# Kernel optimization log

Hardware: AMD Instinct MI355X
Metric: run time of the kernel (lower is better)

The kernel has to match this reference:

```python
import jax, jax.numpy as jnp
import numpy as np

NUM_HEADS = 16
DIM = 1024
HARMONICS = 32
B, L = 2, 2048


def holo_linear(x, basis, phase, amp):
    # x: [B,L,in]; basis: [H,in] (L2-normalized rows); phase/amp: [out,H]
    # Original builds complex(res,0) * amp*exp(i*phase) and takes real of sum
    # over harmonics -> sum_h res_h * amp[o,h]*cos(phase[o,h]).
    resonance = jnp.einsum('bli,hi->blh', x, basis)        # [B,L,H]
    w = amp * jnp.cos(phase)                               # [out,H]
    return jnp.einsum('blh,oh->blo', resonance, w)         # [B,L,out]


def setup_inputs() -> dict:
    key = jax.random.key(0)
    ks = jax.random.split(key, 13)
    two_pi = 2.0 * np.pi

    def make_proj(k0, k1):
        basis = jax.random.normal(k0, (HARMONICS, DIM), dtype=jnp.float32)
        basis = basis / jnp.linalg.norm(basis, axis=1, keepdims=True)
        phase = jax.random.normal(k1, (DIM, HARMONICS), dtype=jnp.float32) * two_pi
        amp = jnp.ones((DIM, HARMONICS), dtype=jnp.float32) / HARMONICS
        return basis, phase, amp

    x = jax.random.normal(ks[0], (B, L, DIM), dtype=jnp.float32)
    bq, pq, aq = make_proj(ks[1], ks[2])
    bk, pk, ak = make_proj(ks[3], ks[4])
    bv, pv, av = make_proj(ks[5], ks[6])
    bo, po, ao = make_proj(ks[7], ks[8])
    return {
        'x': x,
        'basis_q': bq, 'phase_q': pq, 'amp_q': aq,
        'basis_k': bk, 'phase_k': pk, 'amp_k': ak,
        'basis_v': bv, 'phase_v': pv, 'amp_v': av,
        'basis_o': bo, 'phase_o': po, 'amp_o': ao,
    }


def reference(x, basis_q, phase_q, amp_q, basis_k, phase_k, amp_k,
              basis_v, phase_v, amp_v, basis_o, phase_o, amp_o):
    Bsz, Ls, C = x.shape
    head_dim = C // NUM_HEADS
    scale = head_dim ** (-0.5)

    def split_heads(t):  # [B,L,C] -> [B,H,L,hd]
        return t.reshape(Bsz, Ls, NUM_HEADS, head_dim).transpose(0, 2, 1, 3)

    q = split_heads(holo_linear(x, basis_q, phase_q, amp_q))
    k = split_heads(holo_linear(x, basis_k, phase_k, amp_k))
    v = split_heads(holo_linear(x, basis_v, phase_v, amp_v))

    attn = jnp.einsum('bhqd,bhkd->bhqk', q, k) * scale      # [B,H,L,L]
    attn = jax.nn.softmax(attn, axis=-1)
    out = jnp.einsum('bhqk,bhkd->bhqd', attn, v)            # [B,H,L,hd]
    out = out.transpose(0, 2, 1, 3).reshape(Bsz, Ls, C)
    return holo_linear(out, basis_o, phase_o, amp_o)
```

## Files before the change

kernel.cpp:

```cpp
#include <hip/hip_runtime.h>
#include <hip/hip_bf16.h>
#include <cstdint>
#include <cstddef>

#define NH   16
#define HD   64
#define CD   1024
#define HARM 32
#define BSZ  2
#define LSEQ 2048
#define NROW (BSZ*LSEQ)

typedef __attribute__((ext_vector_type(8))) short short8;
typedef __attribute__((ext_vector_type(16))) float float16v;

__device__ inline ushort bf16u(float f) {
    __hip_bfloat16 h = __float2bfloat16(f);
    return *(ushort*)&h;
}
__device__ inline float ubf(ushort u) {
    return __uint_as_float((unsigned)u << 16);
}
__device__ inline unsigned pk2(float a, float b) {
    return (unsigned)bf16u(a) | ((unsigned)bf16u(b) << 16);
}
__device__ inline int crow(int r, int half) { return (r & 3) + 8 * (r >> 2) + 4 * half; }

union S8U { short8 v; uint2 u[2]; };

__device__ inline short8 pk_frag(const unsigned* pk, int cc) {
    S8U o;
    o.u[0] = make_uint2(pk[4 * cc + 0], pk[4 * cc + 1]);
    o.u[1] = make_uint2(pk[4 * cc + 2], pk[4 * cc + 3]);
    return o.v;
}

__global__ void prep_kern(const float* __restrict__ bq, const float* __restrict__ bk,
                          const float* __restrict__ bv, const float* __restrict__ bo,
                          const float* __restrict__ pq, const float* __restrict__ aq,
                          const float* __restrict__ pk, const float* __restrict__ ak,
                          const float* __restrict__ pv, const float* __restrict__ av,
                          const float* __restrict__ po, const float* __restrict__ ao,
                          ushort* __restrict__ bF, ushort* __restrict__ wqkvF,
                          ushort* __restrict__ wobF) {
    const float QSCALE = 0.125f * 1.44269504088896340736f;
    unsigned tid = blockIdx.x * 256 + threadIdx.x;
    if (tid < 16384) {
        unsigned l31 = tid & 31, h = (tid >> 5) & 1, kc = (tid >> 6) & 63, proj = tid >> 12;
        const float* bp = (proj == 0) ? bq : (proj == 1) ? bk : (proj == 2) ? bv : bo;
        const float* s = bp + (size_t)l31 * CD + kc * 16;
        unsigned o0 = (proj == 3) ? h * 4 : h * 8;
        unsigned o1 = o0 + ((proj == 3) ? 8 : 4);
        float4 f0 = *(const float4*)(s + o0), f1 = *(const float4*)(s + o1);
        S8U o;
        o.u[0] = make_uint2(pk2(f0.x, f0.y), pk2(f0.z, f0.w));
        o.u[1] = make_uint2(pk2(f1.x, f1.y), pk2(f1.z, f1.w));
        *(short8*)(bF + (size_t)tid * 8) = o.v;
        return;
    }
    if (tid < 28672) {
        unsigned i = tid - 16384;
        unsigned l31 = i & 31, h = (i >> 5) & 1, kc2 = (i >> 6) & 1;
        unsigned ntp = (i >> 7) & 31, proj = i >> 12;
        const float* ph = (proj == 0) ? pq : (proj == 1) ? pk : pv;
        const float* am = (proj == 0) ? aq : (proj == 1) ? ak : av;
        float sc = (proj == 0) ? QSCALE : 1.0f;
        size_t s = (size_t)(ntp * 32 + l31) * HARM + kc2 * 16 + h * 4;
        float4 p0 = *(const float4*)(ph + s), p1 = *(const float4*)(ph + s + 8);
        float4 a0 = *(const float4*)(am + s), a1 = *(const float4*)(am + s + 8);
        S8U o;
        o.u[0] = make_uint2(pk2(a0.x * cosf(p0.x) * sc, a0.y * cosf(p0.y) * sc),
                            pk2(a0.z * cosf(p0.z) * sc, a0.w * cosf(p0.w) * sc));
        o.u[1] = make_uint2(pk2(a1.x * cosf(p1.x) * sc, a1.y * cosf(p1.y) * sc),
                            pk2(a1.z * cosf(p1.z) * sc, a1.w * cosf(p1.w) * sc));
        *(short8*)(wqkvF + (size_t)i * 8) = o.v;
        return;
    }
    {
        unsigned i = tid - 28672;
        unsigned l31 = i & 31, h = (i >> 5) & 1, kc2 = (i >> 6) & 1, nt = i >> 7;
        size_t s = (size_t)(nt * 32 + l31) * HARM + kc2 * 16 + h * 4;
        float4 p0 = *(const float4*)(po + s), p1 = *(const float4*)(po + s + 8);
        float4 a0 = *(const float4*)(ao + s), a1 = *(const float4*)(ao + s + 8);
        S8U o;
        o.u[0] = make_uint2(pk2(a0.x * cosf(p0.x), a0.y * cosf(p0.y)),
                            pk2(a0.z * cosf(p0.z), a0.w * cosf(p0.w)));
        o.u[1] = make_uint2(pk2(a1.x * cosf(p1.x), a1.y * cosf(p1.y)),
                            pk2(a1.z * cosf(p1.z), a1.w * cosf(p1.w)));
        *(short8*)(wobF + (size_t)i * 8) = o.v;
    }
}

__global__ __launch_bounds__(512) void resrp_kern(const float* __restrict__ x,
                                                  const ushort* __restrict__ bF,
                                                  unsigned* __restrict__ rfbuf) {
    __shared__ ushort xs[4][8192];
    float* red = (float*)xs;
    const int t = threadIdx.x, wave = t >> 6, lane = t & 63;
    const int l31 = lane & 31, h = lane >> 5;
    const int rest = blockIdx.x;
    const int n0 = rest * 32;

#pragma unroll
    for (int i = 0; i < 16; i++) {
        int idx = i * 512 + t;
        int row = idx >> 8, c4g = idx & 255;
        int kseg = c4g >> 6, c4 = c4g & 63;
        float4 v = *(const float4*)(x + (size_t)(n0 + row) * CD + kseg * 256 + c4 * 4);
        int chunk = (c4 >> 1) ^ (row & 15), sub = c4 & 1;
        *(ushort4*)(&xs[kseg][row * 256 + chunk * 8 + sub * 4]) =
            make_ushort4(bf16u(v.x), bf16u(v.y), bf16u(v.z), bf16u(v.w));
    }
    __syncthreads();

    float16v resC[3] = {};
#pragma unroll
    for (int i = 0; i < 8; i++) {
        int kcg = wave * 8 + i;
        int kseg = kcg >> 4, m = kcg & 15;
        int c = m * 2 + h;
        short8 bx = *(const short8*)(&xs[kseg][l31 * 256 + ((c ^ (l31 & 15)) * 8)]);
#pragma unroll
        for (int p = 0; p < 3; p++) {
            short8 a = *(const short8*)(bF + ((size_t)((p * 64 + kcg) * 2 + h) * 32 + l31) * 8);
            resC[p] = __builtin_amdgcn_mfma_f32_32x32x16_bf16(a, bx, resC[p], 0, 0, 0);
        }
    }

    unsigned* ob = rfbuf + (size_t)rest * 1536;
    for (int p = 0; p < 3; p++) {
        __syncthreads();
#pragma unroll
        for (int r = 0; r < 16; r++) red[wave * 1024 + r * 64 + lane] = resC[p][r];
        __syncthreads();
        if (t < 128) {
            int cc = t >> 6, ln = t & 63;
            unsigned w[4];
#pragma unroll
            for (int q = 0; q < 4; q++) {
                int j = cc * 4 + q;
                float va = 0.0f, vb2 = 0.0f;
#pragma unroll
                for (int wv = 0; wv < 8; wv++) {
                    va  += red[wv * 1024 + (2 * j) * 64 + ln];
                    vb2 += red[wv * 1024 + (2 * j + 1) * 64 + ln];
                }
                w[q] = pk2(va, vb2);
            }
            *(uint4*)(ob + ((p * 2 + cc) * 64 + ln) * 4) =
                make_uint4(w[0], w[1], w[2], w[3]);
        }
    }
}

__global__ __launch_bounds__(256) void qkv_kern(const unsigned* __restrict__ rfbuf,
                                                const ushort* __restrict__ wqkvF,
                                                ushort* __restrict__ qtile,
                                                ushort* __restrict__ ktile,
                                                ushort* __restrict__ vtile) {
    const int t = threadIdx.x, wave = t >> 6, lane = t & 63;
    const int l31 = lane & 31, h = lane >> 5;
    const int ntg = blockIdx.x % 24, rest = blockIdx.x / 24;
    const int b = rest >> 6, l0q = rest & 63;
    const int nt = ntg * 4 + wave;
    const int proj = nt >> 5, ntp = nt & 31;
    const int head = ntp >> 1, sub = ntp & 1;
    const int kblk = l0q >> 1, mtk = l0q & 1;

    const unsigned* rb = rfbuf + (size_t)rest * 1536 + ((proj * 2) * 64 + lane) * 4;
    uint4 q0 = *(const uint4*)(rb);
    uint4 q1 = *(const uint4*)(rb + 256);
    S8U r0, r1;
    r0.u[0] = make_uint2(q0.x, q0.y); r0.u[1] = make_uint2(q0.z, q0.w);
    r1.u[0] = make_uint2(q1.x, q1.y); r1.u[1] = make_uint2(q1.z, q1.w);

    const ushort* wp = wqkvF + ((size_t)(proj * 32 + ntp) * 4) * 256;
    short8 wf0 = *(const short8*)(wp + (size_t)h * 256 + l31 * 8);
    short8 wf1 = *(const short8*)(wp + (size_t)(2 + h) * 256 + l31 * 8);
    float16v c = {};
    if (proj < 2) {
        c = __builtin_amdgcn_mfma_f32_32x32x16_bf16(wf0, r0.v, c, 0, 0, 0);
        c = __builtin_amdgcn_mfma_f32_32x32x16_bf16(wf1, r1.v, c, 0, 0, 0);
    } else {
        c = __builtin_amdgcn_mfma_f32_32x32x16_bf16(r0.v, wf0, c, 0, 0, 0);
        c = __builtin_amdgcn_mfma_f32_32x32x16_bf16(r1.v, wf1, c, 0, 0, 0);
    }
    unsigned pkc[8];
#pragma unroll
    for (int j = 0; j < 8; j++) pkc[j] = pk2(c[2 * j], c[2 * j + 1]);

    if (proj == 0) {
        ushort* base = qtile + (((size_t)(b * NH + head) * 64 + l0q)) * 2048;
#pragma unroll
        for (int cc = 0; cc < 2; cc++)
            *(short8*)(base + (sub * 2 + cc) * 512 + h * 256 + l31 * 8) =
                pk_frag(pkc, cc);
    } else if (proj == 1) {
        ushort* base = ktile + ((size_t)(b * NH + head) * 32 + kblk) * 4096 + mtk * 2048;
#pragma unroll
        for (int cc = 0; cc < 2; cc++)
            *(short8*)(base + (sub * 2 + cc) * 512 + h * 256 + l31 * 8) =
                pk_frag(pkc, cc);
    } else {
        ushort* base = vtile + ((size_t)(b * NH + head) * 32 + kblk) * 4096 + sub * 2048;
#pragma unroll
        for (int cc = 0; cc < 2; cc++)
            *(short8*)(base + (mtk * 2 + cc) * 512 + h * 256 + l31 * 8) =
                pk_frag(pkc, cc);
    }
}

__global__ __launch_bounds__(256, 2) void flash8(const ushort* __restrict__ qtile,
                                                 const ushort* __restrict__ ktile,
                                                 const ushort* __restrict__ vtile,
                                                 ushort* __restrict__ Opart,
                                                 float* __restrict__ lbuf) {
    __shared__ ushort kb[2][4096];
    __shared__ ushort vb[2][4096];
    const int t = threadIdx.x;
    const int wave = t >> 6, lane = t & 63;
    const int l31 = lane & 31, h = lane >> 5;
    const int d = blockIdx.x;
    const int logical = (d & 7) * 64 + (d >> 3);
    const int bh = logical >> 4;
    const int inner = logical & 15;
    const int ksp = inner >> 3;
    const int qtg = inner & 7;
    const int qt0 = qtg * 8 + wave * 2;
    const int fo = h * 256 + l31 * 8;
    const int so = t * 8;

    const ushort* qtb = qtile + ((size_t)bh * 64 + qt0) * 2048;
    short8 qfa[4], qfb[4];
#pragma unroll
    for (int kc = 0; kc < 4; kc++) {
        qfa[kc] = *(const short8*)(qtb + kc * 512 + fo);
        qfb[kc] = *(const short8*)(qtb + 2048 + kc * 512 + fo);
    }

    const ushort* ktb = ktile + (size_t)bh * 32 * 4096;
    const ushort* vtb = vtile + (size_t)bh * 32 * 4096;
    const int k0 = ksp * 16;

    {
        const ushort* ks = ktb + (size_t)k0 * 4096;
        const ushort* vs = vtb + (size_t)k0 * 4096;
        short8 a0 = *(const short8*)(ks + so);
        short8 a1 = *(const short8*)(ks + 2048 + so);
        short8 b0 = *(const short8*)(vs + so);
        short8 b1 = *(const short8*)(vs + 2048 + so);
        *(short8*)(kb[0] + so) = a0; *(short8*)(kb[0] + 2048 + so) = a1;
        *(short8*)(vb[0] + so) = b0; *(short8*)(vb[0] + 2048 + so) = b1;
    }
    __syncthreads();

    S8U ones;
    ones.u[0] = make_uint2(0x3F803F80u, 0x3F803F80u);
    ones.u[1] = make_uint2(0x3F803F80u, 0x3F803F80u);

    float16v O0a = {}, O1a = {}, Laa = {};
    float16v O0b = {}, O1b = {}, Lab = {};

#pragma unroll
    for (int it = 0; it < 16; it++) {
        const int cur = it & 1, nxt = cur ^ 1;

        short8 a0, a1, b0, b1;
        if (it < 15) {
            const ushort* ks = ktb + (size_t)(k0 + it + 1) * 4096;
            const ushort* vs = vtb + (size_t)(k0 + it + 1) * 4096;
            a0 = *(const short8*)(ks + so);
            a1 = *(const short8*)(ks + 2048 + so);
            b0 = *(const short8*)(vs + so);
            b1 = *(const short8*)(vs + 2048 + so);
        }

        short8 kf[2][4];
#pragma unroll
        for (int mt = 0; mt < 2; mt++)
#pragma unroll
            for (int kc = 0; kc < 4; kc++)
                kf[mt][kc] = *(const short8*)(kb[cur] + mt * 2048 + kc * 512 + fo);
        float16v s0a = {}, s1a = {}, s0b = {}, s1b = {};
#pragma unroll
        for (int kc = 0; kc < 4; kc++) {
            s0a = __builtin_amdgcn_mfma_f32_32x32x16_bf16(kf[0][kc], qfa[kc], s0a, 0, 0, 0);
            s1a = __builtin_amdgcn_mfma_f32_32x32x16_bf16(kf[1][kc], qfa[kc], s1a, 0, 0, 0);
            s0b = __builtin_amdgcn_mfma_f32_32x32x16_bf16(kf[0][kc], qfb[kc], s0b, 0, 0, 0);
            s1b = __builtin_amdgcn_mfma_f32_32x32x16_bf16(kf[1][kc], qfb[kc], s1b, 0, 0, 0);
        }
        short8 vf[2][4];
#pragma unroll
        for (int mt = 0; mt < 2; mt++)
#pragma unroll
            for (int kc = 0; kc < 4; kc++)
                vf[mt][kc] = *(const short8*)(vb[cur] + mt * 2048 + kc * 512 + fo);

        unsigned pk0a[8], pk1a[8], pk0b[8], pk1b[8];
#pragma unroll
        for (int j2 = 0; j2 < 8; j2++) {
            pk0a[j2] = pk2(__builtin_amdgcn_exp2f(s0a[2 * j2]),
                           __builtin_amdgcn_exp2f(s0a[2 * j2 + 1]));
            pk1a[j2] = pk2(__builtin_amdgcn_exp2f(s1a[2 * j2]),
                           __builtin_amdgcn_exp2f(s1a[2 * j2 + 1]));
            pk0b[j2] = pk2(__builtin_amdgcn_exp2f(s0b[2 * j2]),
                           __builtin_amdgcn_exp2f(s0b[2 * j2 + 1]));
            pk1b[j2] = pk2(__builtin_amdgcn_exp2f(s1b[2 * j2]),
                           __builtin_amdgcn_exp2f(s1b[2 * j2 + 1]));
        }
#pragma unroll
        for (int kc = 0; kc < 4; kc++) {
            const unsigned* pma = (kc < 2) ? pk0a : pk1a;
            const unsigned* pmb = (kc < 2) ? pk0b : pk1b;
            short8 bfa = pk_frag(pma, kc & 1);
            short8 bfb = pk_frag(pmb, kc & 1);
            Laa = __builtin_amdgcn_mfma_f32_32x32x16_bf16(ones.v, bfa, Laa, 0, 0, 0);
            O0a = __builtin_amdgcn_mfma_f32_32x32x16_bf16(vf[0][kc], bfa, O0a, 0, 0, 0);
            O1a = __builtin_amdgcn_mfma_f32_32x32x16_bf16(vf[1][kc], bfa, O1a, 0, 0, 0);
            Lab = __builtin_amdgcn_mfma_f32_32x32x16_bf16(ones.v, bfb, Lab, 0, 0, 0);
            O0b = __builtin_amdgcn_mfma_f32_32x32x16_bf16(vf[0][kc], bfb, O0b, 0, 0, 0);
            O1b = __builtin_amdgcn_mfma_f32_32x32x16_bf16(vf[1][kc], bfb, O1b, 0, 0, 0);
        }

        if (it < 15) {
            *(short8*)(kb[nxt] + so) = a0; *(short8*)(kb[nxt] + 2048 + so) = a1;
            *(short8*)(vb[nxt] + so) = b0; *(short8*)(vb[nxt] + 2048 + so) = b1;
        }
        __syncthreads();
    }

    if (h == 0) {
        lbuf[(size_t)ksp * 65536 + bh * 2048 + qt0 * 32 + l31] = Laa[0];
        lbuf[(size_t)ksp * 65536 + bh * 2048 + (qt0 + 1) * 32 + l31] = Lab[0];
    }
#pragma unroll
    for (int j = 0; j < 2; j++) {
        ushort* ob = Opart + (size_t)ksp * 4194304 + ((size_t)bh * 64 + qt0 + j) * 2048;
#pragma unroll
        for (int mt = 0; mt < 2; mt++) {
            float16v Ov = j ? (mt ? O1b : O0b) : (mt ? O1a : O0a);
            unsigned pkO[8];
#pragma unroll
            for (int j2 = 0; j2 < 8; j2++) pkO[j2] = pk2(Ov[2 * j2], Ov[2 * j2 + 1]);
#pragma unroll
            for (int cc = 0; cc < 2; cc++)
                *(short8*)(ob + ((mt * 2 + cc) * 2 + h) * 256 + l31 * 8) =
                    pk_frag(pkO, cc);
        }
    }
}

__global__ __launch_bounds__(256) void back1_kern(const ushort* __restrict__ Opart,
                                                  const float* __restrict__ lbuf,
                                                  const ushort* __restrict__ bF,
                                                  float* __restrict__ respart2) {
    __shared__ float red[4 * 16 * 64];
    const int t = threadIdx.x, wave = t >> 6, lane = t & 63;
    const int l31 = lane & 31, h = lane >> 5;
    const int hq = blockIdx.x & 3, rg = blockIdx.x >> 2;
    const int b = rg >> 6, qt = rg & 63;
    const int hd = hq * 4 + wave, bh = b * NH + hd;

    float lb = lbuf[(size_t)bh * 2048 + qt * 32 + l31] +
               lbuf[(size_t)65536 + (size_t)bh * 2048 + qt * 32 + l31];
    float invl = 1.0f / lb;
    const ushort* ob0 = Opart + ((size_t)bh * 64 + qt) * 2048;
    const ushort* ob1 = ob0 + 4194304;

    float16v c = {};
#pragma unroll
    for (int kc = 0; kc < 4; kc++) {
        short8 o0 = *(const short8*)(ob0 + (kc * 2 + h) * 256 + l31 * 8);
        short8 o1 = *(const short8*)(ob1 + (kc * 2 + h) * 256 + l31 * 8);
        float av[8];
#pragma unroll
        for (int e = 0; e < 8; e++)
            av[e] = (ubf((ushort)o0[e]) + ubf((ushort)o1[e])) * invl;
        S8U bn;
        bn.u[0] = make_uint2(pk2(av[0], av[1]), pk2(av[2], av[3]));
        bn.u[1] = make_uint2(pk2(av[4], av[5]), pk2(av[6], av[7]));
        int kcg = hd * 4 + kc;
        short8 a = *(const short8*)(bF + ((size_t)((3 * 64 + kcg) * 2 + h) * 32 + l31) * 8);
        c = __builtin_amdgcn_mfma_f32_32x32x16_bf16(a, bn.v, c, 0, 0, 0);
    }
#pragma unroll
    for (int r = 0; r < 16; r++) red[wave * 1024 + r * 64 + lane] = c[r];
    __syncthreads();
#pragma unroll
    for (int i = 0; i < 4; i++) {
        int e = i * 256 + t;
        respart2[((size_t)hq * 128 + rg) * 1024 + e] =
            (red[e] + red[1024 + e]) + (red[2048 + e] + red[3072 + e]);
    }
}

__global__ __launch_bounds__(256) void back2_kern(const float* __restrict__ respart2,
                                                  const ushort* __restrict__ wobF,
                                                  float* __restrict__ out) {
    const int t = threadIdx.x, wave = t >> 6, lane = t & 63;
    const int l31 = lane & 31, h = lane >> 5;
    const int ng = blockIdx.x & 7, rg = blockIdx.x >> 3;

    float cf[16];
#pragma unroll
    for (int r = 0; r < 16; r++) {
        const float* pp = respart2 + r * 64 + lane;
        cf[r] = (pp[(size_t)rg * 1024] + pp[(size_t)(128 + rg) * 1024]) +
                (pp[(size_t)(256 + rg) * 1024] + pp[(size_t)(384 + rg) * 1024]);
    }
    unsigned pkr[8];
#pragma unroll
    for (int j = 0; j < 8; j++) pkr[j] = pk2(cf[2 * j], cf[2 * j + 1]);
    short8 a0 = pk_frag(pkr, 0);
    short8 a1 = pk_frag(pkr, 1);

    int nt = ng * 4 + wave;
    const ushort* wp = wobF + (size_t)nt * 1024;
    short8 wf0 = *(const short8*)(wp + (size_t)h * 256 + l31 * 8);
    short8 wf1 = *(const short8*)(wp + (size_t)(2 + h) * 256 + l31 * 8);
    float16v co = {};
    co = __builtin_amdgcn_mfma_f32_32x32x16_bf16(a0, wf0, co, 0, 0, 0);
    co = __builtin_amdgcn_mfma_f32_32x32x16_bf16(a1, wf1, co, 0, 0, 0);
#pragma unroll
    for (int r = 0; r < 16; r++) {
        int row = rg * 32 + crow(r, h);
        out[(size_t)row * CD + nt * 32 + l31] = co[r];
    }
}

extern "C" void kernel_launch(void* const* d_in, const int* in_sizes, int n_in,
                              void* d_out, int out_size, void* d_ws, size_t ws_size,
                              hipStream_t stream) {
    const float* x  = (const float*)d_in[0];
    const float* bq = (const float*)d_in[1];
    const float* pq = (const float*)d_in[2];
    const float* aq = (const float*)d_in[3];
    const float* bk = (const float*)d_in[4];
    const float* pk = (const float*)d_in[5];
    const float* ak = (const float*)d_in[6];
    const float* bv = (const float*)d_in[7];
    const float* pv = (const float*)d_in[8];
    const float* av = (const float*)d_in[9];
    const float* bo = (const float*)d_in[10];
    const float* po = (const float*)d_in[11];
    const float* ao = (const float*)d_in[12];

    char* ws = (char*)d_ws;
    ushort* bF      = (ushort*)(ws + 0);
    ushort* wqkvF   = (ushort*)(ws + 262144);
    ushort* wobF    = (ushort*)(ws + 458752);
    ushort* qtile   = (ushort*)(ws + 524288);
    ushort* ktile   = (ushort*)(ws + 8912896);
    ushort* vtile   = (ushort*)(ws + 17301504);
    ushort* Opart   = (ushort*)(ws + 25690112);
    float*  lbuf    = (float*)(ws + 42467328);
    float*  respart2= (float*)(ws + 524288);
    unsigned* rfbuf = (unsigned*)(ws + 25690112);

    prep_kern<<<128, 256, 0, stream>>>(bq, bk, bv, bo, pq, aq, pk, ak, pv, av,
                                       po, ao, bF, wqkvF, wobF);
    resrp_kern<<<128, 512, 0, stream>>>(x, bF, rfbuf);
    qkv_kern<<<3072, 256, 0, stream>>>(rfbuf, wqkvF, qtile, ktile, vtile);
    flash8<<<512, 256, 0, stream>>>(qtile, ktile, vtile, Opart, lbuf);
    back1_kern<<<512, 256, 0, stream>>>(Opart, lbuf, bF, respart2);
    back2_kern<<<1024, 256, 0, stream>>>(respart2, wobF, (float*)d_out);
}
```

Measured before the change: 151.7 us.

## Fuse back-projection kernels into one 1024-thread block per row tile

New measurement: 148.3 us. -2.2%, faster.

```diff
diff --git a/kernel.cpp b/kernel.cpp
--- a/kernel.cpp
+++ b/kernel.cpp
@@ -350,16 +350,18 @@
     }
 }
 
-__global__ __launch_bounds__(256) void back1_kern(const ushort* __restrict__ Opart,
-                                                  const float* __restrict__ lbuf,
-                                                  const ushort* __restrict__ bF,
-                                                  float* __restrict__ respart2) {
-    __shared__ float red[4 * 16 * 64];
+__global__ __launch_bounds__(1024) void backf_kern(const ushort* __restrict__ Opart,
+                                                   const float* __restrict__ lbuf,
+                                                   const ushort* __restrict__ bF,
+                                                   const ushort* __restrict__ wobF,
+                                                   float* __restrict__ out) {
+    __shared__ float red[16 * 1024];
+    __shared__ unsigned pkrL[512];
     const int t = threadIdx.x, wave = t >> 6, lane = t & 63;
     const int l31 = lane & 31, h = lane >> 5;
-    const int hq = blockIdx.x & 3, rg = blockIdx.x >> 2;
+    const int rg = blockIdx.x;
     const int b = rg >> 6, qt = rg & 63;
-    const int hd = hq * 4 + wave, bh = b * NH + hd;
+    const int bh = b * NH + wave;
 
     float lb = lbuf[(size_t)bh * 2048 + qt * 32 + l31] +
                lbuf[(size_t)65536 + (size_t)bh * 2048 + qt * 32 + l31];
@@ -379,52 +381,54 @@
         S8U bn;
         bn.u[0] = make_uint2(pk2(av[0], av[1]), pk2(av[2], av[3]));
         bn.u[1] = make_uint2(pk2(av[4], av[5]), pk2(av[6], av[7]));
-        int kcg = hd * 4 + kc;
+        int kcg = wave * 4 + kc;
         short8 a = *(const short8*)(bF + ((size_t)((3 * 64 + kcg) * 2 + h) * 32 + l31) * 8);
         c = __builtin_amdgcn_mfma_f32_32x32x16_bf16(a, bn.v, c, 0, 0, 0);
     }
 #pragma unroll
     for (int r = 0; r < 16; r++) red[wave * 1024 + r * 64 + lane] = c[r];
     __syncthreads();
-#pragma unroll
-    for (int i = 0; i < 4; i++) {
-        int e = i * 256 + t;
-        respart2[((size_t)hq * 128 + rg) * 1024 + e] =
-            (red[e] + red[1024 + e]) + (red[2048 + e] + red[3072 + e]);
-    }
-}
-
-__global__ __launch_bounds__(256) void back2_kern(const float* __restrict__ respart2,
-                                                  const ushort* __restrict__ wobF,
-                                                  float* __restrict__ out) {
-    const int t = threadIdx.x, wave = t >> 6, lane = t & 63;
-    const int l31 = lane & 31, h = lane >> 5;
-    const int ng = blockIdx.x & 7, rg = blockIdx.x >> 3;
-
-    float cf[16];
-#pragma unroll
-    for (int r = 0; r < 16; r++) {
-        const float* pp = respart2 + r * 64 + lane;
-        cf[r] = (pp[(size_t)rg * 1024] + pp[(size_t)(128 + rg) * 1024]) +
-                (pp[(size_t)(256 + rg) * 1024] + pp[(size_t)(384 + rg) * 1024]);
-    }
+
+    if (t < 512) {
+        int j = t >> 6, ln = t & 63;
+        float cf2[2];
+#pragma unroll
+        for (int s2 = 0; s2 < 2; s2++) {
+            int off = (2 * j + s2) * 64 + ln;
+            float hq0 = (red[0 * 1024 + off] + red[1 * 1024 + off]) +
+                        (red[2 * 1024 + off] + red[3 * 1024 + off]);
+            float hq1 = (red[4 * 1024 + off] + red[5 * 1024 + off]) +
+                        (red[6 * 1024 + off] + red[7 * 1024 + off]);
+            float hq2 = (red[8 * 1024 + off] + red[9 * 1024 + off]) +
+                        (red[10 * 1024 + off] + red[11 * 1024 + off]);
+            float hq3 = (red[12 * 1024 + off] + red[13 * 1024 + off]) +
+                        (red[14 * 1024 + off] + red[15 * 1024 + off]);
+            cf2[s2] = (hq0 + hq1) + (hq2 + hq3);
+        }
+        pkrL[j * 64 + ln] = pk2(cf2[0], cf2[1]);
+    }
+    __syncthreads();
+
     unsigned pkr[8];
 #pragma unroll
-    for (int j = 0; j < 8; j++) pkr[j] = pk2(cf[2 * j], cf[2 * j + 1]);
+    for (int j = 0; j < 8; j++) pkr[j] = pkrL[j * 64 + lane];
     short8 a0 = pk_frag(pkr, 0);
     short8 a1 = pk_frag(pkr, 1);
 
-    int nt = ng * 4 + wave;
-    const ushort* wp = wobF + (size_t)nt * 1024;
-    short8 wf0 = *(const short8*)(wp + (size_t)h * 256 + l31 * 8);
-    short8 wf1 = *(const short8*)(wp + (size_t)(2 + h) * 256 + l31 * 8);
-    float16v co = {};
-    co = __builtin_amdgcn_mfma_f32_32x32x16_bf16(a0, wf0, co, 0, 0, 0);
-    co = __builtin_amdgcn_mfma_f32_32x32x16_bf16(a1, wf1, co, 0, 0, 0);
-#pragma unroll
-    for (int r = 0; r < 16; r++) {
-        int row = rg * 32 + crow(r, h);
-        out[(size_t)row * CD + nt * 32 + l31] = co[r];
+#pragma unroll
+    for (int i = 0; i < 2; i++) {
+        int nt = wave * 2 + i;
+        const ushort* wp = wobF + (size_t)nt * 1024;
+        short8 wf0 = *(const short8*)(wp + (size_t)h * 256 + l31 * 8);
+        short8 wf1 = *(const short8*)(wp + (size_t)(2 + h) * 256 + l31 * 8);
+        float16v co = {};
+        co = __builtin_amdgcn_mfma_f32_32x32x16_bf16(a0, wf0, co, 0, 0, 0);
+        co = __builtin_amdgcn_mfma_f32_32x32x16_bf16(a1, wf1, co, 0, 0, 0);
+#pragma unroll
+        for (int r = 0; r < 16; r++) {
+            int row = rg * 32 + crow(r, h);
+            out[(size_t)row * CD + nt * 32 + l31] = co[r];
+        }
     }
 }
 
@@ -454,7 +458,6 @@
     ushort* vtile   = (ushort*)(ws + 17301504);
     ushort* Opart   = (ushort*)(ws + 25690112);
     float*  lbuf    = (float*)(ws + 42467328);
-    float*  respart2= (float*)(ws + 524288);
     unsigned* rfbuf = (unsigned*)(ws + 25690112);
 
     prep_kern<<<128, 256, 0, stream>>>(bq, bk, bv, bo, pq, aq, pk, ak, pv, av,
@@ -462,6 +465,5 @@
     resrp_kern<<<128, 512, 0, stream>>>(x, bF, rfbuf);
     qkv_kern<<<3072, 256, 0, stream>>>(rfbuf, wqkvF, qtile, ktile, vtile);
     flash8<<<512, 256, 0, stream>>>(qtile, ktile, vtile, Opart, lbuf);
-    back1_kern<<<512, 256, 0, stream>>>(Opart, lbuf, bF, respart2);
-    back2_kern<<<1024, 256, 0, stream>>>(respart2, wobF, (float*)d_out);
-}
+    backf_kern<<<128, 1024, 0, stream>>>(Opart, lbuf, bF, wobF, (float*)d_out);
+}
```
